# Kernel tuning notes

Hardware: AMD Instinct MI355X
Metric: run time of the kernel (lower is better)

Reference implementation:

```python
import jax, jax.numpy as jnp
import numpy as np
from jax import lax

DIM = 192
NUM_CLASSES = 4
D_INNER = 2 * DIM          # expand=2
D_STATE = 16
D_CONV = 4
DT_RANK = (DIM + 15) // 16  # ceil(192/16)=12
PATCH = 16


def _mamba_params(key, prefix):
    ks = jax.random.split(key, 9)
    s = lambda k, shape, scale: (jax.random.normal(k, shape, jnp.float32) * scale)
    p = {
        prefix + '_in_w':   s(ks[0], (2 * D_INNER, DIM), 0.02),
        prefix + '_conv_w': s(ks[1], (D_INNER, D_CONV), 0.1),
        prefix + '_conv_b': jnp.zeros((D_INNER,), jnp.float32),
        prefix + '_xproj_w': s(ks[2], (DT_RANK + 2 * D_STATE, D_INNER), 0.02),
        prefix + '_dt_w':   s(ks[3], (D_INNER, DT_RANK), 0.1),
        prefix + '_dt_b':   s(ks[4], (D_INNER,), 0.1),
        # A_log init: log(1..d_state) broadcast over d_inner (mamba default)
        prefix + '_A_log':  jnp.broadcast_to(jnp.log(jnp.arange(1, D_STATE + 1, dtype=jnp.float32)), (D_INNER, D_STATE)) + 0.0,
        prefix + '_D':      jnp.ones((D_INNER,), jnp.float32),
        prefix + '_out_w':  s(ks[5], (DIM, D_INNER), 0.02),
    }
    return p


def setup_inputs() -> dict:
    key = jax.random.key(0)
    ks = jax.random.split(key, 8)
    inp = {
        'x': jax.random.normal(ks[0], (32, 3, 384, 384), jnp.float32),
        'patch_w': jax.random.normal(ks[1], (DIM, 3, PATCH, PATCH), jnp.float32) * 0.02,
        'patch_b': jnp.zeros((DIM,), jnp.float32),
        'ln_g': jnp.ones((DIM,), jnp.float32),
        'ln_b': jnp.zeros((DIM,), jnp.float32),
        'fc_w': jax.random.normal(ks[2], (NUM_CLASSES, DIM), jnp.float32) * 0.02,
        'fc_b': jnp.zeros((NUM_CLASSES,), jnp.float32),
    }
    inp.update(_mamba_params(ks[3], 'f'))
    inp.update(_mamba_params(ks[4], 'b'))
    return inp


def _layernorm(x, g, b, eps=1e-5):
    mu = jnp.mean(x, -1, keepdims=True)
    var = jnp.mean(jnp.square(x - mu), -1, keepdims=True)
    return (x - mu) * lax.rsqrt(var + eps) * g + b


def _mamba(x, in_w, conv_w, conv_b, xproj_w, dt_w, dt_b, A_log, Dskip, out_w):
    # x: [B, L, DIM]
    Bn, L, _ = x.shape
    xz = x @ in_w.T                                    # [B, L, 2*di]
    xi, z = jnp.split(xz, 2, axis=-1)
    # causal depthwise conv1d, kernel D_CONV, left pad
    xp = jnp.pad(xi, ((0, 0), (D_CONV - 1, 0), (0, 0)))
    xc = conv_b + sum(xp[:, k:k + L, :] * conv_w[:, k] for k in range(D_CONV))
    xc = jax.nn.silu(xc)                               # [B, L, di]
    proj = xc @ xproj_w.T                              # [B, L, dtr+2*ds]
    dt, Bm, Cm = jnp.split(proj, [DT_RANK, DT_RANK + D_STATE], axis=-1)
    dt = jax.nn.softplus(dt @ dt_w.T + dt_b)           # [B, L, di]
    A = -jnp.exp(A_log)                                # [di, ds]

    def step(h, inp):
        dt_t, B_t, C_t, x_t = inp                      # [B,di],[B,ds],[B,ds],[B,di]
        dA = jnp.exp(dt_t[:, :, None] * A)             # [B, di, ds]
        h = dA * h + (dt_t * x_t)[:, :, None] * B_t[:, None, :]
        y = jnp.einsum('bds,bs->bd', h, C_t)
        return h, y

    h0 = jnp.zeros((Bn, D_INNER, D_STATE), x.dtype)
    xs = (dt.transpose(1, 0, 2), Bm.transpose(1, 0, 2),
          Cm.transpose(1, 0, 2), xc.transpose(1, 0, 2))
    _, ys = lax.scan(step, h0, xs)                     # [L, B, di]
    y = ys.transpose(1, 0, 2) + xc * Dskip
    y = y * jax.nn.silu(z)
    return y @ out_w.T                                 # [B, L, DIM]


def reference(x, patch_w, patch_b, ln_g, ln_b, fc_w, fc_b,
              f_in_w, f_conv_w, f_conv_b, f_xproj_w, f_dt_w, f_dt_b, f_A_log, f_D, f_out_w,
              b_in_w, b_conv_w, b_conv_b, b_xproj_w, b_dt_w, b_dt_b, b_A_log, b_D, b_out_w):
    Bn, C, H, W = x.shape
    Hp, Wp = H // PATCH, W // PATCH
    # patch embed: stride==kernel conv == reshape + einsum
    xr = x.reshape(Bn, C, Hp, PATCH, Wp, PATCH)
    tok = jnp.einsum('bchpwq,dcpq->bhwd', xr, patch_w) + patch_b
    tok = tok.reshape(Bn, Hp * Wp, DIM)                # [B, L, D]
    tok = _layernorm(tok, ln_g, ln_b)
    fwd = _mamba(tok, f_in_w, f_conv_w, f_conv_b, f_xproj_w, f_dt_w, f_dt_b, f_A_log, f_D, f_out_w)
    bwd = _mamba(tok[:, ::-1, :], b_in_w, b_conv_w, b_conv_b, b_xproj_w, b_dt_w, b_dt_b, b_A_log, b_D, b_out_w)
    out = fwd + bwd[:, ::-1, :]
    pooled = jnp.mean(out, axis=1)                     # adaptive avg pool to 1
    return pooled @ fc_w.T + fc_b                      # [B, num_classes]
```

## Files before the change

### kernel.cpp

```cpp
#include <hip/hip_runtime.h>
#include <hip/hip_bf16.h>

#define NC 32
#define CL 18

typedef __attribute__((ext_vector_type(8))) short short8;
typedef __attribute__((ext_vector_type(4))) float f32x4;
typedef __attribute__((ext_vector_type(2))) float f32x2;

__device__ __forceinline__ float sigm(float x){ return 1.0f/(1.0f+__expf(-x)); }

__device__ __forceinline__ ushort f2bf(float f){
  unsigned u = __float_as_uint(f);
  unsigned r = (u + 0x7fffu + ((u>>16)&1u)) >> 16;
  return (ushort)r;
}
__device__ __forceinline__ float bf2f(ushort h){ return __uint_as_float(((unsigned)h)<<16); }

__global__ __launch_bounds__(256) void k_prep_all(
    const float* __restrict__ patch_w, const float* __restrict__ f_in_w,
    const float* __restrict__ b_in_w,
    const float* __restrict__ f_xw, const float* __restrict__ b_xw,
    const float* __restrict__ f_cw, const float* __restrict__ b_cw,
    const float* __restrict__ f_al, const float* __restrict__ b_al,
    const float* __restrict__ fc_w, const float* __restrict__ f_ow,
    const float* __restrict__ b_ow,
    ushort* __restrict__ pw_h, ushort* __restrict__ pw_l,
    ushort* __restrict__ iw_h, ushort* __restrict__ iw_l,
    ushort* __restrict__ xw_h, ushort* __restrict__ xw_l,
    float* __restrict__ cwT, float* __restrict__ Abuf,
    float* __restrict__ A0fl, float* __restrict__ W2){
  const int bx = blockIdx.x, t = threadIdx.x;
  if (bx < 1728){
    int which = bx/576;
    int i = (bx - which*576)*256 + t;
    if (which==0){
      float f = patch_w[i];
      ushort hb = f2bf(f);
      pw_h[i]=hb; pw_l[i]=f2bf(f - bf2f(hb));
    } else {
      const float* src = (which==1) ? f_in_w : b_in_w;
      int dirofs = (which==1) ? 0 : 48;
      float f = src[i];
      int n = i/192, k = i%192;
      int nblk = n>>4, r = n&15, kblk = k>>5, kk = k&31;
      int lane = r + ((kk>>3)<<4), j = kk&7;
      size_t idx = ((size_t)((nblk+dirofs)*6 + kblk)*64 + lane)*8 + j;
      ushort hb = f2bf(f);
      iw_h[idx]=hb; iw_l[idx]=f2bf(f - bf2f(hb));
    }
  } else if (bx < 1872){
    int i = (bx-1728)*256 + t;
    int dir=i/(48*384), rem=i%(48*384), n=rem/384, k=rem%384;
    float v = (n<44) ? (dir?b_xw:f_xw)[n*384+k] : 0.f;
    ushort hb = f2bf(v);
    xw_h[i]=hb; xw_l[i]=f2bf(v - bf2f(hb));
  } else if (bx < 1884){
    int i = (bx-1872)*256 + t;
    int dir=i/1536, rem=i%1536, j=rem/384, k=rem%384;
    cwT[i] = (dir ? b_cw : f_cw)[k*4+j];
  } else if (bx < 1887){
    int i = (bx-1884)*256 + t;
    if (i < 768){
      int dir=i/384, di=i%384;
      const float* alp = (dir?b_al:f_al) + di*16;
      float A0 = -expf(alp[0]);
      bool fast = true;
      Abuf[(size_t)i*16] = A0;
      #pragma unroll
      for (int s=1;s<16;s++){
        float A = -expf(alp[s]);
        Abuf[(size_t)i*16+s] = A;
        fast = fast && (fabsf(A - (s+1)*A0) <= 1e-5f*(s+1)*fabsf(A0));
      }
      A0fl[i*2]=A0; A0fl[i*2+1]=fast?1.f:0.f;
    }
  } else {
    int i = (bx-1887)*256 + t;
    if (i < 768){
      int dir=i/384, di=i%384;
      const float* ow = dir ? b_ow : f_ow;
      float a0=0.f,a1=0.f,a2=0.f,a3=0.f;
      for (int d=0; d<192; ++d){
        float o = ow[d*384 + di];
        a0 += fc_w[0*192+d]*o; a1 += fc_w[1*192+d]*o;
        a2 += fc_w[2*192+d]*o; a3 += fc_w[3*192+d]*o;
      }
      W2[(0*2+dir)*384+di]=a0; W2[(1*2+dir)*384+di]=a1;
      W2[(2*2+dir)*384+di]=a2; W2[(3*2+dir)*384+di]=a3;
    }
  }
}
__device__ __forceinline__ float w2at(const float* W2, int dir, int ch, int di){
  return W2[(ch*2+dir)*384+di];
}

__global__ __launch_bounds__(1024) void k_patch(
    const float* __restrict__ x,
    const ushort* __restrict__ pw_h, const ushort* __restrict__ pw_l,
    const float* __restrict__ pb, const float* __restrict__ lng,
    const float* __restrict__ lnb,
    ushort* __restrict__ tokf_h, ushort* __restrict__ tokf_l,
    int b0, int Mc){
  __shared__ __align__(16) char sBmem[49152];
  __shared__ __align__(16) ushort sAh[64*64], sAl[64*64];
  __shared__ float sLN[4][64][2];
  ushort* sBh = (ushort*)sBmem;
  ushort* sBl = (ushort*)(sBmem + 24576);
  const int tid = threadIdx.x;
  const int m0 = blockIdx.x*64;
  const int lane = tid&63, w = tid>>6;
  const int wr = w>>2, wc = w&3;
  const int r = lane&15, g = lane>>4;
  f32x4 acc[3];
  #pragma unroll
  for (int i=0;i<3;i++) acc[i] = (f32x4){0.f,0.f,0.f,0.f};

  for (int s=0;s<12;s++){
    const int c = s>>2, p0 = (s&3)*4;
    {
      int f = tid;
      int m = f>>4, rem = f&15, pp = rem>>2, qq = rem&3;
      int rm = m0 + m;
      float4 v = make_float4(0.f,0.f,0.f,0.f);
      if (rm < Mc){
        int b = b0 + rm/576, l = rm%576, hp = l/24, wp = l%24;
        size_t idx4 = ((size_t)((b*3+c)*384) + hp*16 + p0+pp)*96 + wp*4 + qq;
        v = reinterpret_cast<const float4*>(x)[idx4];
      }
      ushort4 hv, lv;
      hv.x=f2bf(v.x); lv.x=f2bf(v.x-bf2f(hv.x));
      hv.y=f2bf(v.y); lv.y=f2bf(v.y-bf2f(hv.y));
      hv.z=f2bf(v.z); lv.z=f2bf(v.z-bf2f(hv.z));
      hv.w=f2bf(v.w); lv.w=f2bf(v.w-bf2f(hv.w));
      int byte = (m*128 + pp*32 + qq*8) ^ ((m&7)<<4);
      *reinterpret_cast<ushort4*>((char*)sAh + byte) = hv;
      *reinterpret_cast<ushort4*>((char*)sAl + byte) = lv;
    }
    #pragma unroll
    for (int i=0;i<2;i++){
      int f = tid + i*1024;
      if (f < 1536){
        int n = f>>3, k8 = f&7;
        size_t gi = (size_t)n*768 + s*64 + k8*8;
        uint4 bh = *reinterpret_cast<const uint4*>(pw_h + gi);
        uint4 bl = *reinterpret_cast<const uint4*>(pw_l + gi);
        int byte = (n*128 + k8*16) ^ ((n&7)<<4);
        *reinterpret_cast<uint4*>((char*)sBh + byte) = bh;
        *reinterpret_cast<uint4*>((char*)sBl + byte) = bl;
      }
    }
    __syncthreads();
    #pragma unroll
    for (int kk=0;kk<2;kk++){
      int arow = wr*16 + r;
      int abyte = (arow*128 + kk*64 + g*16) ^ ((arow&7)<<4);
      short8 ah = *reinterpret_cast<const short8*>((char*)sAh + abyte);
      short8 al = *reinterpret_cast<const short8*>((char*)sAl + abyte);
      #pragma unroll
      for (int nfl=0; nfl<3; nfl++){
        int brow = (wc*3+nfl)*16 + r;
        int bbyte = (brow*128 + kk*64 + g*16) ^ ((brow&7)<<4);
        short8 bh = *reinterpret_cast<const short8*>((char*)sBh + bbyte);
        short8 bll = *reinterpret_cast<const short8*>((char*)sBl + bbyte);
        acc[nfl] = __builtin_amdgcn_mfma_f32_16x16x32_bf16(ah, bh, acc[nfl], 0,0,0);
        acc[nfl] = __builtin_amdgcn_mfma_f32_16x16x32_bf16(ah, bll, acc[nfl], 0,0,0);
        acc[nfl] = __builtin_amdgcn_mfma_f32_16x16x32_bf16(al, bh, acc[nfl], 0,0,0);
      }
    }
    __syncthreads();
  }
  float pbv[3], gv[3], bv[3];
  #pragma unroll
  for (int nfl=0;nfl<3;nfl++){
    int col = (wc*3+nfl)*16 + r;
    pbv[nfl]=pb[col]; gv[nfl]=lng[col]; bv[nfl]=lnb[col];
  }
  #pragma unroll
  for (int nfl=0;nfl<3;nfl++)
    #pragma unroll
    for (int q=0;q<4;q++) acc[nfl][q] += pbv[nfl];
  float sum[4]={0,0,0,0}, sq[4]={0,0,0,0};
  #pragma unroll
  for (int nfl=0;nfl<3;nfl++)
    #pragma unroll
    for (int q=0;q<4;q++){ float v=acc[nfl][q]; sum[q]+=v; sq[q]+=v*v; }
  #pragma unroll
  for (int off=1; off<16; off<<=1){
    #pragma unroll
    for (int q=0;q<4;q++){
      sum[q]+=__shfl_xor(sum[q],off);
      sq[q] +=__shfl_xor(sq[q],off);
    }
  }
  if (r==0){
    #pragma unroll
    for (int q=0;q<4;q++){
      int row = wr*16 + g*4 + q;
      sLN[wc][row][0]=sum[q]; sLN[wc][row][1]=sq[q];
    }
  }
  __syncthreads();
  float* sT = (float*)sBmem;
  #pragma unroll
  for (int q=0;q<4;q++){
    int rl = wr*16 + g*4 + q;
    float stot = sLN[0][rl][0]+sLN[1][rl][0]+sLN[2][rl][0]+sLN[3][rl][0];
    float qtot = sLN[0][rl][1]+sLN[1][rl][1]+sLN[2][rl][1]+sLN[3][rl][1];
    float mu = stot*(1.f/192.f);
    float var = qtot*(1.f/192.f) - mu*mu;
    float rs = rsqrtf(var + 1e-5f);
    #pragma unroll
    for (int nfl=0;nfl<3;nfl++)
      sT[rl*192 + (wc*3+nfl)*16 + r] = (acc[nfl][q]-mu)*rs*gv[nfl] + bv[nfl];
  }
  __syncthreads();
  const int mB = m0>>4;
  #pragma unroll
  for (int i=0;i<2;i++){
    int fl = tid + 1024*i;
    if (fl < 1536){
      int mb = fl/384, rem = fl-mb*384, kb = rem>>6, ln = rem&63;
      int rr = ln&15, gq = ln>>4;
      const float* sp = sT + (mb*16+rr)*192 + kb*32 + gq*8;
      short8 hv, lv;
      #pragma unroll
      for (int j=0;j<8;j++){
        float v = sp[j];
        ushort hb = f2bf(v);
        hv[j] = (short)hb;
        lv[j] = (short)f2bf(v - bf2f(hb));
      }
      size_t o = ((size_t)((mB+mb)*6 + kb)*64 + ln)*8;
      *reinterpret_cast<short8*>(tokf_h + o) = hv;
      *reinterpret_cast<short8*>(tokf_l + o) = lv;
    }
  }
}

__global__ __launch_bounds__(256) void k_inproj(
    const ushort* __restrict__ tokf_h, const ushort* __restrict__ tokf_l,
    const ushort* __restrict__ iw_h, const ushort* __restrict__ iw_l,
    float* __restrict__ xib, ushort* __restrict__ zb, int Bc, int Mc){
  const int tid = threadIdx.x;
  const int lane = tid&63, w = tid>>6, wr = w>>1, wc = w&1;
  const int r = lane&15, g = lane>>4;
  const int m0 = blockIdx.x*64;
  const int n0 = blockIdx.y*128;
  const int mbase = (m0>>4) + wr*2;
  const int nbase = (n0>>4) + wc*4;
  const bool dir1 = (n0 >= 768);
  const int n0d = dir1 ? n0-768 : n0;
  const bool isZ = (n0d >= 384);
  f32x4 acc[2][4];
  #pragma unroll
  for (int a=0;a<2;a++)
    #pragma unroll
    for (int b=0;b<4;b++) acc[a][b] = (f32x4){0.f,0.f,0.f,0.f};

  if (isZ){
    for (int s=0;s<6;s++){
      short8 ah[2];
      #pragma unroll
      for (int mf=0;mf<2;mf++){
        size_t fi = (((size_t)(mbase+mf)*6 + s)*64 + lane)*8;
        ah[mf] = *reinterpret_cast<const short8*>(tokf_h + fi);
      }
      #pragma unroll
      for (int nf=0;nf<4;nf++){
        size_t fi = (((size_t)(nbase+nf)*6 + s)*64 + lane)*8;
        short8 bh = *reinterpret_cast<const short8*>(iw_h + fi);
        #pragma unroll
        for (int mf=0;mf<2;mf++)
          acc[mf][nf] = __builtin_amdgcn_mfma_f32_16x16x32_bf16(ah[mf], bh, acc[mf][nf], 0,0,0);
      }
    }
  } else {
    for (int s=0;s<6;s++){
      short8 ah[2], al[2];
      #pragma unroll
      for (int mf=0;mf<2;mf++){
        size_t fi = (((size_t)(mbase+mf)*6 + s)*64 + lane)*8;
        ah[mf] = *reinterpret_cast<const short8*>(tokf_h + fi);
        al[mf] = *reinterpret_cast<const short8*>(tokf_l + fi);
      }
      #pragma unroll
      for (int nf=0;nf<4;nf++){
        size_t fi = (((size_t)(nbase+nf)*6 + s)*64 + lane)*8;
        short8 bh = *reinterpret_cast<const short8*>(iw_h + fi);
        short8 bl = *reinterpret_cast<const short8*>(iw_l + fi);
        #pragma unroll
        for (int mf=0;mf<2;mf++){
          acc[mf][nf] = __builtin_amdgcn_mfma_f32_16x16x32_bf16(ah[mf], bh, acc[mf][nf], 0,0,0);
          acc[mf][nf] = __builtin_amdgcn_mfma_f32_16x16x32_bf16(ah[mf], bl, acc[mf][nf], 0,0,0);
          acc[mf][nf] = __builtin_amdgcn_mfma_f32_16x16x32_bf16(al[mf], bh, acc[mf][nf], 0,0,0);
        }
      }
    }
  }
  const int cb = n0d + wc*64;
  #pragma unroll
  for (int mf=0;mf<2;mf++){
    #pragma unroll
    for (int q=0;q<4;q++){
      int rm = m0 + wr*32 + mf*16 + g*4 + q;
      if (rm < Mc){
        size_t row;
        if (dir1){
          int bl = rm/576, l = rm%576;
          row = (size_t)(Bc + bl)*576 + (575-l);
        } else {
          row = (size_t)rm;
        }
        #pragma unroll
        for (int nf=0;nf<4;nf++){
          int col = cb + nf*16;
          float v = acc[mf][nf][q];
          if (isZ){
            v = v*sigm(v);
            zb[row*384 + col-384 + r] = f2bf(v);
          } else {
            xib[row*384 + col + r] = v;
          }
        }
      }
    }
  }
}

__global__ __launch_bounds__(256) void k_convx(
    const float* __restrict__ xib, const float* __restrict__ cwT,
    const float* __restrict__ f_cb, const float* __restrict__ b_cb,
    const ushort* __restrict__ xw_h, const ushort* __restrict__ xw_l,
    float* __restrict__ proj, ushort* __restrict__ xcb, int Bc){
  __shared__ __align__(16) float sRaw[67*64];
  __shared__ __align__(16) ushort sAh[64*64], sAl[64*64];
  __shared__ __align__(16) ushort sBh[48*64], sBl[48*64];
  const int dir = blockIdx.z, blk = blockIdx.y, l0 = blockIdx.x*64;
  const int tid = threadIdx.x, lane = tid&63, w = tid>>6;
  const int r = lane&15, g = lane>>4;
  const size_t seq = ((size_t)dir*Bc + blk)*576;
  const float* cwTd = cwT + dir*1536;
  const float* cbp  = dir?b_cb:f_cb;
  const ushort* bhp = xw_h + dir*48*384;
  const ushort* blp = xw_l + dir*48*384;
  f32x4 acc[3];
  #pragma unroll
  for (int i=0;i<3;i++) acc[i] = (f32x4){0.f,0.f,0.f,0.f};

  for (int kc=0; kc<6; ++kc){
    #pragma unroll
    for (int i=0;i<5;i++){
      int f = tid + i*256;
      if (f < 67*16){
        int rr = f>>4, kq = f&15;
        int l = l0 + rr - 3;
        float4 v = make_float4(0.f,0.f,0.f,0.f);
        if (l >= 0) v = *reinterpret_cast<const float4*>(xib + (seq+l)*384 + kc*64 + kq*4);
        int kqs = kq ^ (rr&15);
        *reinterpret_cast<float4*>(sRaw + rr*64 + kqs*4) = v;
      }
    }
    __syncthreads();
    #pragma unroll
    for (int i=0;i<4;i++){
      int f = tid + i*256;
      int m = f>>4, kq = f&15;
      float4 a = reinterpret_cast<const float4*>(cbp)[kc*16 + kq];
      #pragma unroll
      for (int j=0;j<4;j++){
        int rr = m + j;
        float4 rv = *reinterpret_cast<const float4*>(sRaw + rr*64 + (kq ^ (rr&15))*4);
        float4 cv = reinterpret_cast<const float4*>(cwTd)[j*96 + kc*16 + kq];
        a.x += cv.x*rv.x; a.y += cv.y*rv.y; a.z += cv.z*rv.z; a.w += cv.w*rv.w;
      }
      a.x = a.x*sigm(a.x); a.y = a.y*sigm(a.y); a.z = a.z*sigm(a.z); a.w = a.w*sigm(a.w);
      ushort4 hv, lv;
      hv.x=f2bf(a.x); lv.x=f2bf(a.x-bf2f(hv.x));
      hv.y=f2bf(a.y); lv.y=f2bf(a.y-bf2f(hv.y));
      hv.z=f2bf(a.z); lv.z=f2bf(a.z-bf2f(hv.z));
      hv.w=f2bf(a.w); lv.w=f2bf(a.w-bf2f(hv.w));
      *reinterpret_cast<ushort4*>(xcb + (seq + l0 + m)*384 + kc*64 + kq*4) = hv;
      int byte = (m*128 + kq*8) ^ ((m&7)<<4);
      *reinterpret_cast<ushort4*>((char*)sAh + byte) = hv;
      *reinterpret_cast<ushort4*>((char*)sAl + byte) = lv;
    }
    #pragma unroll
    for (int i=0;i<2;i++){
      int f = tid + i*256;
      if (f < 384){
        int n = f>>3, k8 = f&7;
        size_t gi = (size_t)n*384 + kc*64 + k8*8;
        uint4 vh = *reinterpret_cast<const uint4*>(bhp + gi);
        uint4 vl = *reinterpret_cast<const uint4*>(blp + gi);
        int byte = (n*128 + k8*16) ^ ((n&7)<<4);
        *reinterpret_cast<uint4*>((char*)sBh + byte) = vh;
        *reinterpret_cast<uint4*>((char*)sBl + byte) = vl;
      }
    }
    __syncthreads();
    #pragma unroll
    for (int kk=0;kk<2;kk++){
      int arow = w*16 + r;
      int abyte = (arow*128 + kk*64 + g*16) ^ ((arow&7)<<4);
      short8 ah = *reinterpret_cast<const short8*>((char*)sAh + abyte);
      short8 al = *reinterpret_cast<const short8*>((char*)sAl + abyte);
      #pragma unroll
      for (int nf=0;nf<3;nf++){
        int brow = nf*16 + r;
        int bbyte = (brow*128 + kk*64 + g*16) ^ ((brow&7)<<4);
        short8 bh = *reinterpret_cast<const short8*>((char*)sBh + bbyte);
        short8 bll = *reinterpret_cast<const short8*>((char*)sBl + bbyte);
        acc[nf] = __builtin_amdgcn_mfma_f32_16x16x32_bf16(ah, bh, acc[nf], 0,0,0);
        acc[nf] = __builtin_amdgcn_mfma_f32_16x16x32_bf16(ah, bll, acc[nf], 0,0,0);
        acc[nf] = __builtin_amdgcn_mfma_f32_16x16x32_bf16(al, bh, acc[nf], 0,0,0);
      }
    }
    __syncthreads();
  }
  #pragma unroll
  for (int nf=0;nf<3;nf++){
    int col = nf*16 + r;
    if (col < 44){
      #pragma unroll
      for (int q=0;q<4;q++){
        int l = l0 + w*16 + g*4 + q;
        proj[(seq+l)*44 + col] = acc[nf][q];
      }
    }
  }
}

__global__ __launch_bounds__(256) void k_scan_p1(
    const ushort* __restrict__ zb, const ushort* __restrict__ xcb,
    const float* __restrict__ proj,
    const float* __restrict__ f_dtw, const float* __restrict__ b_dtw,
    const float* __restrict__ f_dtb, const float* __restrict__ b_dtb,
    const float* __restrict__ A0fl, const float* __restrict__ Abuf,
    const float* __restrict__ f_D,  const float* __restrict__ b_D,
    const float* __restrict__ W2, float* __restrict__ dtend,
    float* __restrict__ hbuf, float* __restrict__ part, int b0, int Bc){
  __shared__ float sP[72*44];
  const int dir=blockIdx.z, bl=blockIdx.y;
  const int gg=blockIdx.x>>3, cq=blockIdx.x&7;
  const int wv=threadIdx.x>>6, lane=threadIdx.x&63;
  const int c = cq*4 + wv;
  const int di = gg*64 + lane;
  const size_t seq = ((size_t)dir*Bc + bl)*576;
  {
    const float* src = proj + (seq + (size_t)cq*4*CL)*44;
    #pragma unroll
    for (int i=0;i<13;i++){
      int f = threadIdx.x + i*256;
      if (f < 72*44) sP[f] = src[f];
    }
  }
  __syncthreads();
  const float* dtwp = (dir?b_dtw:f_dtw) + di*12;
  float dtw[12];
  #pragma unroll
  for (int i=0;i<3;i++){
    float4 t = reinterpret_cast<const float4*>(dtwp)[i];
    dtw[4*i]=t.x; dtw[4*i+1]=t.y; dtw[4*i+2]=t.z; dtw[4*i+3]=t.w;
  }
  float dtb = (dir?b_dtb:f_dtb)[di];
  float2 af = reinterpret_cast<const float2*>(A0fl)[dir*384+di];
  const float A0 = af.x;
  const bool fast = (af.y != 0.f);
  float A[16];
  if (!fast){
    #pragma unroll
    for (int s=0;s<16;s++) A[s] = Abuf[((size_t)dir*384+di)*16+s];
  }
  float Dv = (dir?b_D:f_D)[di];
  float w2c[4];
  #pragma unroll
  for (int ch=0;ch<4;ch++) w2c[ch] = w2at(W2,dir,ch,di);
  f32x2 h2[8];
  #pragma unroll
  for (int p=0;p<8;p++) h2[p]=(f32x2){0.f,0.f};
  float S=0.f, cum=0.f;
  const int l0 = c*CL;
  const ushort* xcp = xcb + di;
  const ushort* zbp2 = zb + di;
  for (int j=0;j<CL;j++){
    const size_t row = seq + l0 + j;
    const float* pr = sP + (wv*CL+j)*44;
    const float4* pr4 = reinterpret_cast<const float4*>(pr);
    float4 t0=pr4[0], t1=pr4[1], t2=pr4[2];
    float dtin = dtb
      + t0.x*dtw[0]+t0.y*dtw[1]+t0.z*dtw[2]+t0.w*dtw[3]
      + t1.x*dtw[4]+t1.y*dtw[5]+t1.z*dtw[6]+t1.w*dtw[7]
      + t2.x*dtw[8]+t2.y*dtw[9]+t2.z*dtw[10]+t2.w*dtw[11];
    float dt = (dtin > 20.f) ? dtin : __logf(1.f + __expf(dtin));
    cum += dt;
    float xc = bf2f(xcp[row*384]);
    float zs = bf2f(zbp2[row*384]);
    float u = dt*xc;
    f32x2 u2 = {u,u};
    f32x2 dA2[8];
    if (fast){
      float e1=__expf(dt*A0);
      float e2=e1*e1;
      f32x2 e2v={e2,e2};
      dA2[0]=(f32x2){e1,e2};
      #pragma unroll
      for (int p=1;p<8;p++) dA2[p]=dA2[p-1]*e2v;
    } else {
      #pragma unroll
      for (int p=0;p<8;p++){
        dA2[p]=(f32x2){__expf(dt*A[2*p]), __expf(dt*A[2*p+1])};
      }
    }
    f32x2 ya={0.f,0.f}, yb={0.f,0.f};
    #pragma unroll
    for (int i=0;i<4;i++){
      float4 tb=pr4[3+i], tc=pr4[7+i];
      f32x2 B0={tb.x,tb.y}, B1={tb.z,tb.w};
      f32x2 C0={tc.x,tc.y}, C1={tc.z,tc.w};
      h2[2*i]   = dA2[2*i]*h2[2*i]     + u2*B0;
      h2[2*i+1] = dA2[2*i+1]*h2[2*i+1] + u2*B1;
      ya += h2[2*i]*C0;
      yb += h2[2*i+1]*C1;
    }
    S += ((ya[0]+ya[1])+(yb[0]+yb[1]) + xc*Dv)*zs;
  }
  dtend[(((size_t)dir*Bc + bl)*NC + c)*384 + di] = cum;
  size_t hb = ((((size_t)c*2+dir)*Bc + bl)*6 + gg)*1024;
  #pragma unroll
  for (int s=0;s<16;s++) hbuf[hb + s*64 + lane] = h2[s>>1][s&1];
  float p0=S*w2c[0], p1v=S*w2c[1], p2v=S*w2c[2], p3v=S*w2c[3];
  #pragma unroll
  for (int off=32; off>0; off>>=1){
    p0 += __shfl_xor(p0, off); p1v += __shfl_xor(p1v, off);
    p2v += __shfl_xor(p2v, off); p3v += __shfl_xor(p3v, off);
  }
  if (lane==0){
    float* dst = part + ((((size_t)dir*32 + (b0+bl))*6 + gg)*64 + c)*4;
    dst[0]=p0; dst[1]=p1v; dst[2]=p2v; dst[3]=p3v;
  }
}

__global__ __launch_bounds__(256) void k_combine(
    const float* __restrict__ dtend, float* __restrict__ hbuf,
    const float* __restrict__ A0fl, const float* __restrict__ Abuf, int Bc){
  const int gg=blockIdx.x, bl=blockIdx.y, dir=blockIdx.z;
  const int wv=threadIdx.x>>6, lane=threadIdx.x&63, di=gg*64+lane;
  float2 af = reinterpret_cast<const float2*>(A0fl)[dir*384+di];
  const bool fast = (af.y != 0.f);
  float Aeff[4];
  #pragma unroll
  for (int si=0;si<4;si++){
    int s = wv*4+si;
    Aeff[si] = fast ? af.x*(float)(s+1) : Abuf[((size_t)dir*384+di)*16+s];
  }
  float cur[4];
  size_t hx0 = ((((size_t)0*2+dir)*Bc+bl)*6+gg)*1024 + (wv*4)*64 + lane;
  #pragma unroll
  for (int si=0;si<4;si++) cur[si]=hbuf[hx0 + si*64];
  for (int c=1;c<NC;c++){
    size_t hx=((((size_t)c*2+dir)*Bc+bl)*6+gg)*1024 + (wv*4)*64 + lane;
    float tmp[4];
    #pragma unroll
    for (int si=0;si<4;si++){ tmp[si]=hbuf[hx+si*64]; hbuf[hx+si*64]=cur[si]; }
    if (c<NC-1){
      float Sdt = dtend[(((size_t)dir*Bc+bl)*NC + c)*384 + di];
      #pragma unroll
      for (int si=0;si<4;si++) cur[si] = __expf(Aeff[si]*Sdt)*cur[si] + tmp[si];
    }
  }
}

__global__ __launch_bounds__(256) void k_scan_p2(
    const ushort* __restrict__ zb, const float* __restrict__ proj,
    const float* __restrict__ hbuf,
    const float* __restrict__ f_dtw, const float* __restrict__ b_dtw,
    const float* __restrict__ f_dtb, const float* __restrict__ b_dtb,
    const float* __restrict__ A0fl, const float* __restrict__ Abuf,
    const float* __restrict__ W2, float* __restrict__ part, int b0, int Bc){
  __shared__ float sP[72*44];
  const int dir=blockIdx.z, bl=blockIdx.y;
  const int gg=blockIdx.x>>3, cq=blockIdx.x&7;
  const int wv=threadIdx.x>>6, lane=threadIdx.x&63;
  const int c = cq*4 + wv + 1;
  const int di = gg*64 + lane;
  const size_t seq = ((size_t)dir*Bc + bl)*576;
  {
    const int r0 = (cq*4+1)*CL;
    const float* src = proj + (seq + r0)*44;
    int lim = (576 - r0)*44; if (lim > 72*44) lim = 72*44;
    #pragma unroll
    for (int i=0;i<13;i++){
      int f = threadIdx.x + i*256;
      if (f < lim) sP[f] = src[f];
    }
  }
  __syncthreads();
  if (c >= NC) return;
  const float* dtwp = (dir?b_dtw:f_dtw) + di*12;
  float dtw[12];
  #pragma unroll
  for (int i=0;i<3;i++){
    float4 t = reinterpret_cast<const float4*>(dtwp)[i];
    dtw[4*i]=t.x; dtw[4*i+1]=t.y; dtw[4*i+2]=t.z; dtw[4*i+3]=t.w;
  }
  float dtb = (dir?b_dtb:f_dtb)[di];
  float2 af = reinterpret_cast<const float2*>(A0fl)[dir*384+di];
  const float A0 = af.x;
  const bool fast = (af.y != 0.f);
  float A[16];
  if (!fast){
    #pragma unroll
    for (int s=0;s<16;s++) A[s] = Abuf[((size_t)dir*384+di)*16+s];
  }
  float w2c[4];
  #pragma unroll
  for (int ch=0;ch<4;ch++) w2c[ch]=w2at(W2,dir,ch,di);
  f32x2 hh2[8];
  size_t hb=((((size_t)c*2+dir)*Bc+bl)*6+gg)*1024;
  #pragma unroll
  for (int s=0;s<16;s++) hh2[s>>1][s&1]=hbuf[hb+s*64+lane];
  float S=0.f;
  const int l0 = c*CL;
  const ushort* zbp2 = zb + di;
  for (int j=0;j<CL;j++){
    const size_t row = seq + l0 + j;
    const float* pr = sP + (wv*CL+j)*44;
    const float4* pr4 = reinterpret_cast<const float4*>(pr);
    float4 t0=pr4[0], t1=pr4[1], t2=pr4[2];
    float dtin = dtb
      + t0.x*dtw[0]+t0.y*dtw[1]+t0.z*dtw[2]+t0.w*dtw[3]
      + t1.x*dtw[4]+t1.y*dtw[5]+t1.z*dtw[6]+t1.w*dtw[7]
      + t2.x*dtw[8]+t2.y*dtw[9]+t2.z*dtw[10]+t2.w*dtw[11];
    float dt = (dtin > 20.f) ? dtin : __logf(1.f + __expf(dtin));
    float zs = bf2f(zbp2[row*384]);
    f32x2 dA2[8];
    if (fast){
      float e1=__expf(dt*A0);
      float e2=e1*e1;
      f32x2 e2v={e2,e2};
      dA2[0]=(f32x2){e1,e2};
      #pragma unroll
      for (int p=1;p<8;p++) dA2[p]=dA2[p-1]*e2v;
    } else {
      #pragma unroll
      for (int p=0;p<8;p++){
        dA2[p]=(f32x2){__expf(dt*A[2*p]), __expf(dt*A[2*p+1])};
      }
    }
    f32x2 ya={0.f,0.f}, yb={0.f,0.f};
    #pragma unroll
    for (int i=0;i<4;i++){
      float4 tc = pr4[7+i];
      f32x2 C0={tc.x,tc.y}, C1={tc.z,tc.w};
      hh2[2*i]   = hh2[2*i]*dA2[2*i];
      hh2[2*i+1] = hh2[2*i+1]*dA2[2*i+1];
      ya += hh2[2*i]*C0;
      yb += hh2[2*i+1]*C1;
    }
    S += ((ya[0]+ya[1])+(yb[0]+yb[1]))*zs;
  }
  float p0=S*w2c[0], p1v=S*w2c[1], p2v=S*w2c[2], p3v=S*w2c[3];
  #pragma unroll
  for (int off=32; off>0; off>>=1){
    p0 += __shfl_xor(p0, off); p1v += __shfl_xor(p1v, off);
    p2v += __shfl_xor(p2v, off); p3v += __shfl_xor(p3v, off);
  }
  if (lane==0){
    float* dst = part + ((((size_t)dir*32 + (b0+bl))*6 + gg)*64 + 32 + c)*4;
    dst[0]=p0; dst[1]=p1v; dst[2]=p2v; dst[3]=p3v;
  }
}

__global__ void k_final(const float* __restrict__ part, const float* __restrict__ fc_b,
                        float* __restrict__ out){
  int tid = threadIdx.x;
  if (tid < 128){
    int b = tid>>2, ch = tid&3;
    float s=0.f;
    for (int dir=0;dir<2;dir++)
      for (int g=0;g<6;g++)
        for (int c=0;c<64;c++){
          if (c==32) continue;
          s += part[((((size_t)dir*32 + b)*6 + g)*64 + c)*4 + ch];
        }
    out[b*4+ch] = fc_b[ch] + s*(1.0f/576.0f);
  }
}

extern "C" void kernel_launch(void* const* d_in, const int* in_sizes, int n_in,
                              void* d_out, int out_size, void* d_ws, size_t ws_size,
                              hipStream_t stream){
  const float* x       = (const float*)d_in[0];
  const float* patch_w = (const float*)d_in[1];
  const float* patch_b = (const float*)d_in[2];
  const float* ln_g    = (const float*)d_in[3];
  const float* ln_b    = (const float*)d_in[4];
  const float* fc_w    = (const float*)d_in[5];
  const float* fc_b    = (const float*)d_in[6];
  const float* f_in_w  = (const float*)d_in[7];
  const float* f_cw    = (const float*)d_in[8];
  const float* f_cb    = (const float*)d_in[9];
  const float* f_xw    = (const float*)d_in[10];
  const float* f_dtw   = (const float*)d_in[11];
  const float* f_dtb   = (const float*)d_in[12];
  const float* f_al    = (const float*)d_in[13];
  const float* f_D     = (const float*)d_in[14];
  const float* f_ow    = (const float*)d_in[15];
  const float* b_in_w  = (const float*)d_in[16];
  const float* b_cw    = (const float*)d_in[17];
  const float* b_cb    = (const float*)d_in[18];
  const float* b_xw    = (const float*)d_in[19];
  const float* b_dtw   = (const float*)d_in[20];
  const float* b_dtb   = (const float*)d_in[21];
  const float* b_al    = (const float*)d_in[22];
  const float* b_D     = (const float*)d_in[23];
  const float* b_ow    = (const float*)d_in[24];
  float* out = (float*)d_out;
  float* ws  = (float*)d_ws;

  float* W2    = ws;
  float* part  = W2 + 3072;
  ushort* pw_h = (ushort*)(part + 98304);
  ushort* pw_l = pw_h + 147456;
  ushort* iw_h = pw_l + 147456;
  ushort* iw_l = iw_h + 294912;
  ushort* xw_h = iw_l + 294912;
  ushort* xw_l = xw_h + 36864;
  float* cwT   = (float*)(xw_l + 36864);
  float* Abuf  = cwT + 3072;
  float* A0fl  = Abuf + 12288;
  float* base  = A0fl + 1536;

  const size_t FIXED = 3072 + 98304 + 2*73728 + 2*147456 + 2*18432 + 3072
                     + 12288 + 1536;
  const size_t perB = 110592ull + 442368ull + 110592ull + 110592ull
                    + 24576ull + 393216ull;
  int Bc = 32;
  while (Bc > 1 && (FIXED + (size_t)Bc*perB)*4ull > ws_size) Bc >>= 1;

  ushort* tokf_h = (ushort*)base;
  ushort* tokf_l = tokf_h + (size_t)Bc*110592ull;
  float* prj  = base;
  float* xib  = base + (size_t)Bc*110592ull;
  ushort* zbp = (ushort*)(xib + (size_t)Bc*442368ull);
  ushort* xcb = zbp + (size_t)Bc*442368ull;
  float* dtnd = (float*)(xcb + (size_t)Bc*442368ull);
  float* hbf  = dtnd + (size_t)Bc*24576ull;

  k_prep_all<<<dim3(1890),dim3(256),0,stream>>>(patch_w, f_in_w, b_in_w,
                                                f_xw, b_xw, f_cw, b_cw,
                                                f_al, b_al, fc_w, f_ow, b_ow,
                                                pw_h, pw_l, iw_h, iw_l,
                                                xw_h, xw_l, cwT, Abuf, A0fl, W2);

  for (int b0=0; b0<32; b0+=Bc){
    const int Mc = Bc*576;
    k_patch<<<dim3((Mc+63)/64),dim3(1024),0,stream>>>(x, pw_h, pw_l, patch_b,
                                                      ln_g, ln_b, tokf_h, tokf_l, b0, Mc);
    k_inproj<<<dim3((Mc+63)/64,12),dim3(256),0,stream>>>(tokf_h, tokf_l, iw_h, iw_l,
                                                         xib, zbp, Bc, Mc);
    k_convx<<<dim3(9,Bc,2),dim3(256),0,stream>>>(xib, cwT, f_cb, b_cb,
                                                 xw_h, xw_l, prj, xcb, Bc);
    k_scan_p1<<<dim3(48,Bc,2),dim3(256),0,stream>>>(zbp, xcb, prj,
                                                    f_dtw,b_dtw, f_dtb,b_dtb,
                                                    A0fl, Abuf, f_D,b_D,
                                                    W2, dtnd, hbf, part, b0, Bc);
    k_combine<<<dim3(6,Bc,2),dim3(256),0,stream>>>(dtnd, hbf, A0fl, Abuf, Bc);
    k_scan_p2<<<dim3(48,Bc,2),dim3(256),0,stream>>>(zbp, prj, hbf,
                                                    f_dtw,b_dtw, f_dtb,b_dtb,
                                                    A0fl, Abuf, W2, part, b0, Bc);
  }
  k_final<<<dim3(1),dim3(128),0,stream>>>(part, fc_b, out);
}
```

Measured before the change: 270.5 us.

## Stage in-projection GEMM tiles in LDS with 1024-thread 128x128 blocks

The in-projection GEMM kernel now uses 1024-thread blocks computing 128x128 output tiles. A and B fragments (hi/lo bf16 splits) are cooperatively loaded into shared memory and reused across waves, where before each wave read them from global memory on its own. The epilogue transposes accumulators through shared memory so rows are written with vectorized stores of fp32 xi or bf16 silu(z). This cuts redundant global loads and scattered stores, but adds block-wide barriers and halves the number of blocks, which lowers grid parallelism.

```diff
diff --git a/kernel.cpp b/kernel.cpp
--- a/kernel.cpp
+++ b/kernel.cpp
@@ -238,90 +238,120 @@
   }
 }
 
-__global__ __launch_bounds__(256) void k_inproj(
+__global__ __launch_bounds__(1024) void k_inproj(
     const ushort* __restrict__ tokf_h, const ushort* __restrict__ tokf_l,
     const ushort* __restrict__ iw_h, const ushort* __restrict__ iw_l,
     float* __restrict__ xib, ushort* __restrict__ zb, int Bc, int Mc){
+  __shared__ __align__(16) char sMem[65536];
+  ushort* sAh = (ushort*)sMem;
+  ushort* sAl = (ushort*)(sMem + 16384);
+  ushort* sBh = (ushort*)(sMem + 32768);
+  ushort* sBl = (ushort*)(sMem + 49152);
   const int tid = threadIdx.x;
-  const int lane = tid&63, w = tid>>6, wr = w>>1, wc = w&1;
+  const int lane = tid&63, w = tid>>6;
+  const int wr = w>>2, wc = w&3;
   const int r = lane&15, g = lane>>4;
-  const int m0 = blockIdx.x*64;
-  const int n0 = blockIdx.y*128;
-  const int mbase = (m0>>4) + wr*2;
-  const int nbase = (n0>>4) + wc*4;
-  const bool dir1 = (n0 >= 768);
-  const int n0d = dir1 ? n0-768 : n0;
-  const bool isZ = (n0d >= 384);
-  f32x4 acc[2][4];
+  const int m0 = blockIdx.x*128;
+  const int mb0 = blockIdx.x*8;
+  const int nb0 = blockIdx.y*8;
+  const int n0d = (blockIdx.y%6)*128;
+  const bool dir1 = (blockIdx.y >= 6);
+  const bool isZ = ((blockIdx.y%6) >= 3);
+
+  f32x4 acc[2][2];
   #pragma unroll
   for (int a=0;a<2;a++)
     #pragma unroll
-    for (int b=0;b<4;b++) acc[a][b] = (f32x4){0.f,0.f,0.f,0.f};
-
-  if (isZ){
-    for (int s=0;s<6;s++){
-      short8 ah[2];
+    for (int b=0;b<2;b++) acc[a][b] = (f32x4){0.f,0.f,0.f,0.f};
+
+  for (int s=0;s<3;s++){
+    {
+      const int f = w;
+      const int mf = f>>1, kk = f&1;
+      const size_t ga = ((size_t)((mb0+mf)*6 + 2*s+kk)*64 + lane)*8;
+      const size_t gb = ((size_t)((nb0+mf)*6 + 2*s+kk)*64 + lane)*8;
+      const int so = f*512 + lane*8;
+      *reinterpret_cast<short8*>(sAh+so) = *reinterpret_cast<const short8*>(tokf_h+ga);
+      *reinterpret_cast<short8*>(sBh+so) = *reinterpret_cast<const short8*>(iw_h+gb);
+      if (!isZ){
+        *reinterpret_cast<short8*>(sAl+so) = *reinterpret_cast<const short8*>(tokf_l+ga);
+        *reinterpret_cast<short8*>(sBl+so) = *reinterpret_cast<const short8*>(iw_l+gb);
+      }
+    }
+    __syncthreads();
+    #pragma unroll
+    for (int kk=0;kk<2;kk++){
+      short8 ah[2], al[2];
       #pragma unroll
       for (int mf=0;mf<2;mf++){
-        size_t fi = (((size_t)(mbase+mf)*6 + s)*64 + lane)*8;
-        ah[mf] = *reinterpret_cast<const short8*>(tokf_h + fi);
-      }
-      #pragma unroll
-      for (int nf=0;nf<4;nf++){
-        size_t fi = (((size_t)(nbase+nf)*6 + s)*64 + lane)*8;
-        short8 bh = *reinterpret_cast<const short8*>(iw_h + fi);
+        const int fo = ((wr*2+mf)*2+kk)*512 + lane*8;
+        ah[mf] = *reinterpret_cast<const short8*>(sAh+fo);
+        if (!isZ) al[mf] = *reinterpret_cast<const short8*>(sAl+fo);
+      }
+      #pragma unroll
+      for (int nf=0;nf<2;nf++){
+        const int fo = ((wc*2+nf)*2+kk)*512 + lane*8;
+        short8 bh = *reinterpret_cast<const short8*>(sBh+fo);
+        if (isZ){
+          #pragma unroll
+          for (int mf=0;mf<2;mf++)
+            acc[mf][nf] = __builtin_amdgcn_mfma_f32_16x16x32_bf16(ah[mf], bh, acc[mf][nf], 0,0,0);
+        } else {
+          short8 bl = *reinterpret_cast<const short8*>(sBl+fo);
+          #pragma unroll
+          for (int mf=0;mf<2;mf++){
+            acc[mf][nf] = __builtin_amdgcn_mfma_f32_16x16x32_bf16(ah[mf], bh, acc[mf][nf], 0,0,0);
+            acc[mf][nf] = __builtin_amdgcn_mfma_f32_16x16x32_bf16(ah[mf], bl, acc[mf][nf], 0,0,0);
+            acc[mf][nf] = __builtin_amdgcn_mfma_f32_16x16x32_bf16(al[mf], bh, acc[mf][nf], 0,0,0);
+          }
+        }
+      }
+    }
+    __syncthreads();
+  }
+
+  float* sT = reinterpret_cast<float*>(sMem);
+  const int h_of_w = wr>>1;
+  #pragma unroll
+  for (int h=0; h<2; h++){
+    if (h==1) __syncthreads();
+    if (h_of_w == h){
+      #pragma unroll
+      for (int mf=0;mf<2;mf++)
         #pragma unroll
-        for (int mf=0;mf<2;mf++)
-          acc[mf][nf] = __builtin_amdgcn_mfma_f32_16x16x32_bf16(ah[mf], bh, acc[mf][nf], 0,0,0);
-      }
-    }
-  } else {
-    for (int s=0;s<6;s++){
-      short8 ah[2], al[2];
-      #pragma unroll
-      for (int mf=0;mf<2;mf++){
-        size_t fi = (((size_t)(mbase+mf)*6 + s)*64 + lane)*8;
-        ah[mf] = *reinterpret_cast<const short8*>(tokf_h + fi);
-        al[mf] = *reinterpret_cast<const short8*>(tokf_l + fi);
-      }
-      #pragma unroll
-      for (int nf=0;nf<4;nf++){
-        size_t fi = (((size_t)(nbase+nf)*6 + s)*64 + lane)*8;
-        short8 bh = *reinterpret_cast<const short8*>(iw_h + fi);
-        short8 bl = *reinterpret_cast<const short8*>(iw_l + fi);
-        #pragma unroll
-        for (int mf=0;mf<2;mf++){
-          acc[mf][nf] = __builtin_amdgcn_mfma_f32_16x16x32_bf16(ah[mf], bh, acc[mf][nf], 0,0,0);
-          acc[mf][nf] = __builtin_amdgcn_mfma_f32_16x16x32_bf16(ah[mf], bl, acc[mf][nf], 0,0,0);
-          acc[mf][nf] = __builtin_amdgcn_mfma_f32_16x16x32_bf16(al[mf], bh, acc[mf][nf], 0,0,0);
-        }
-      }
-    }
-  }
-  const int cb = n0d + wc*64;
-  #pragma unroll
-  for (int mf=0;mf<2;mf++){
-    #pragma unroll
-    for (int q=0;q<4;q++){
-      int rm = m0 + wr*32 + mf*16 + g*4 + q;
+        for (int nf=0;nf<2;nf++)
+          #pragma unroll
+          for (int q=0;q<4;q++){
+            int rl = (wr&1)*32 + mf*16 + g*4 + q;
+            int c  = wc*32 + nf*16 + r;
+            sT[rl*132 + c] = acc[mf][nf][q];
+          }
+    }
+    __syncthreads();
+    {
+      const int rl = tid>>4, cg = tid&15;
+      const int rm = m0 + h*64 + rl;
       if (rm < Mc){
         size_t row;
         if (dir1){
-          int bl = rm/576, l = rm%576;
+          int bl = rm/576, l = rm - bl*576;
           row = (size_t)(Bc + bl)*576 + (575-l);
         } else {
           row = (size_t)rm;
         }
-        #pragma unroll
-        for (int nf=0;nf<4;nf++){
-          int col = cb + nf*16;
-          float v = acc[mf][nf][q];
-          if (isZ){
+        const float* sp = sT + rl*132 + cg*8;
+        if (!isZ){
+          *reinterpret_cast<f32x4*>(xib + row*384 + n0d + cg*8)     = *reinterpret_cast<const f32x4*>(sp);
+          *reinterpret_cast<f32x4*>(xib + row*384 + n0d + cg*8 + 4) = *reinterpret_cast<const f32x4*>(sp+4);
+        } else {
+          short8 hv;
+          #pragma unroll
+          for (int j=0;j<8;j++){
+            float v = sp[j];
             v = v*sigm(v);
-            zb[row*384 + col-384 + r] = f2bf(v);
-          } else {
-            xib[row*384 + col + r] = v;
+            hv[j] = (short)f2bf(v);
           }
+          *reinterpret_cast<short8*>(zb + row*384 + (n0d-384) + cg*8) = hv;
         }
       }
     }
@@ -758,8 +788,8 @@
     const int Mc = Bc*576;
     k_patch<<<dim3((Mc+63)/64),dim3(1024),0,stream>>>(x, pw_h, pw_l, patch_b,
                                                       ln_g, ln_b, tokf_h, tokf_l, b0, Mc);
-    k_inproj<<<dim3((Mc+63)/64,12),dim3(256),0,stream>>>(tokf_h, tokf_l, iw_h, iw_l,
-                                                         xib, zbp, Bc, Mc);
+    k_inproj<<<dim3((Mc+127)/128,12),dim3(1024),0,stream>>>(tokf_h, tokf_l, iw_h, iw_l,
+                                                            xib, zbp, Bc, Mc);
     k_convx<<<dim3(9,Bc,2),dim3(256),0,stream>>>(xib, cwT, f_cb, b_cb,
                                                  xw_h, xw_l, prj, xcb, Bc);
     k_scan_p1<<<dim3(48,Bc,2),dim3(256),0,stream>>>(zbp, xcb, prj,
```

Result: no change. 267.5 us (-1.1%).
